# Performance work log

Measured on AMD Instinct MI355X. Metric: run time of the kernel, lower is better.

## Reference

```python
import jax, jax.numpy as jnp
import numpy as np

B, Nq, Nk, R = 4, 1024, 1024, 256
NH, DK, DV = 8, 64, 64


def setup_inputs() -> dict:
    key = jax.random.key(0)
    ks = jax.random.split(key, 16)
    mk = lambda k, shape, s=1.0: jax.random.normal(k, shape, dtype=jnp.float32) * s
    inp = {
        'Q_real': mk(ks[0], (B, Nq, R)), 'Q_imag': mk(ks[1], (B, Nq, R)),
        'K_real': mk(ks[2], (B, Nk, R)), 'K_imag': mk(ks[3], (B, Nk, R)),
        'V_real': mk(ks[4], (B, Nk, R)), 'V_imag': mk(ks[5], (B, Nk, R)),
        'WQ_r': mk(ks[6], (NH * DK, R), 0.02), 'WQ_i': mk(ks[7], (NH * DK, R), 0.02),
        'WK_r': mk(ks[8], (NH * DK, R), 0.02), 'WK_i': mk(ks[9], (NH * DK, R), 0.02),
        'WV_r': mk(ks[10], (NH * DV, R), 0.02), 'WV_i': mk(ks[11], (NH * DV, R), 0.02),
        'WO_r': mk(ks[12], (R, NH * DV), 0.02), 'WO_i': mk(ks[13], (R, NH * DV), 0.02),
        'mask': jax.random.randint(ks[14], (B, Nk), 0, 2).astype(bool),
    }
    return inp


def _complex_linear(x, w_r, w_i):
    # x: complex [..., in]; weights real [out, in]. Same math as 4 real matmuls.
    w = (w_r + 1j * w_i).astype(jnp.complex64)
    return x @ w.T


def reference(Q_real, Q_imag, K_real, K_imag, V_real, V_imag,
              WQ_r, WQ_i, WK_r, WK_i, WV_r, WV_i, WO_r, WO_i, mask):
    Q = (Q_real + 1j * Q_imag).astype(jnp.complex64)
    K = (K_real + 1j * K_imag).astype(jnp.complex64)
    V = (V_real + 1j * V_imag).astype(jnp.complex64)

    Qp = _complex_linear(Q, WQ_r, WQ_i).reshape(B, Nq, NH, DK).transpose(0, 2, 1, 3)
    Kp = _complex_linear(K, WK_r, WK_i).reshape(B, Nk, NH, DK).transpose(0, 2, 1, 3)
    Vp = _complex_linear(V, WV_r, WV_i).reshape(B, Nk, NH, DV).transpose(0, 2, 1, 3)

    # complex scores [B, NH, Nq, Nk]; conj on K matches torch .conj().transpose
    scores = jnp.einsum('bhqd,bhkd->bhqk', Qp, jnp.conj(Kp)) / jnp.sqrt(jnp.float32(DK))
    scores_abs = jnp.abs(scores)

    m = mask[:, None, None, :]                    # [B,1,1,Nk]
    valid = jnp.any(mask, axis=-1)[:, None, None, None]  # [B,1,1,1] valid query rows
    masked = jnp.where(m, scores_abs, -jnp.inf)
    # avoid all -inf rows feeding softmax (those rows are zeroed afterwards)
    safe = jnp.where(valid, masked, 0.0)
    w = jax.nn.softmax(safe, axis=-1)
    w = jnp.where(valid, w, 0.0)

    attn = jnp.einsum('bhqk,bhkd->bhqd', w.astype(Vp.dtype), Vp)
    attn = attn.transpose(0, 2, 1, 3).reshape(B, Nq, NH * DV)
    return _complex_linear(attn, WO_r, WO_i)
```

## Files before the change

### kernel.cpp

```cpp
#include <hip/hip_runtime.h>
#include <math.h>

#define NBATCH 4
#define NSEQ   1024
#define RD     256
#define NHEAD  8
#define HD     64
#define NHD    512

typedef __attribute__((ext_vector_type(8))) short  short8;
typedef __attribute__((ext_vector_type(4))) short  short4v;
typedef __attribute__((ext_vector_type(4))) float  float4v;

#define MFMA16(a,b,c) __builtin_amdgcn_mfma_f32_16x16x32_bf16(a,b,c,0,0,0)

typedef const void __attribute__((address_space(1)))* gas_t;
typedef void __attribute__((address_space(3)))* las_t;
#define GLOAD16(g, l) __builtin_amdgcn_global_load_lds((gas_t)(g), (las_t)(l), 16, 0, 0)

static __device__ __forceinline__ unsigned short f2b(float f) {
    union { float f; unsigned u; } x; x.f = f;
    unsigned r = x.u + 0x7fffu + ((x.u >> 16) & 1u);
    return (unsigned short)(r >> 16);
}
static __device__ __forceinline__ void st4(short* dst, float4v v) {
    short4v p;
    p[0] = (short)f2b(v[0]); p[1] = (short)f2b(v[1]);
    p[2] = (short)f2b(v[2]); p[3] = (short)f2b(v[3]);
    *(short4v*)dst = p;
}

struct ConvArgs { const float* src[15]; short* dst[15]; int n4[15]; };

__global__ __launch_bounds__(256) void convert_bf16(ConvArgs ca)
{
    const int a = blockIdx.y;
    if (a == 14) {
        if (blockIdx.x != 0) return;
        __shared__ int isByteLayout;
        const int t = threadIdx.x;
        if (t == 0) isByteLayout = 0;
        __syncthreads();
        const int* mi = (const int*)ca.src[14];
        #pragma unroll
        for (int j = 0; j < 4; j++) {
            int v = mi[t*4 + j];
            if (v & ~1) isByteLayout = 1;
        }
        __syncthreads();
        unsigned char* nm = (unsigned char*)ca.dst[14];
        const unsigned char* mb = (const unsigned char*)ca.src[14];
        if (isByteLayout) {
            #pragma unroll
            for (int j = 0; j < 16; j++) { int k = t*16 + j; nm[k] = mb[k] ? 1 : 0; }
        } else {
            #pragma unroll
            for (int j = 0; j < 16; j++) { int k = t*16 + j; nm[k] = mi[k] ? 1 : 0; }
        }
        return;
    }
    const float* __restrict__ s = ca.src[a];
    short* __restrict__ d = ca.dst[a];
    const int n4 = ca.n4[a];
    for (int i = blockIdx.x*256 + threadIdx.x; i < n4; i += gridDim.x*256) {
        float4v v = *(const float4v*)(s + (size_t)i*4);
        st4(d + (size_t)i*4, v);
    }
}

struct ProjArgs {
    const short* Xr[3]; const short* Xi[3];
    const short* Wr[3]; const short* Wi[3];
    short* Yr[3]; short* Yi[3];
};

__global__ __launch_bounds__(256) void cgemm_proj(ProjArgs pa)
{
    __shared__ short sX[2][128][64];
    __shared__ short sW[2][64][64];
    const int z = blockIdx.z;
    const short* __restrict__ X_r = pa.Xr[z];
    const short* __restrict__ X_i = pa.Xi[z];
    const short* __restrict__ W_r = pa.Wr[z];
    const short* __restrict__ W_i = pa.Wi[z];
    short* __restrict__ Y_r = pa.Yr[z];
    short* __restrict__ Y_i = pa.Yi[z];
    const int transposeOut = (z == 2);

    const int tid  = threadIdx.x;
    const int lane = tid & 63, wave = tid >> 6;
    const int quad = lane >> 4, l16 = lane & 15;
    const int sw8  = l16 & 7;
    const int rsub = lane >> 3;
    const int colg = (lane & 7) ^ rsub;
    const int n0 = blockIdx.x * 64, m0 = blockIdx.y * 128;

    const short nk = (short)0x8000;
    const short8 neg = {nk,nk,nk,nk,nk,nk,nk,nk};

    float4v zf = {0.f,0.f,0.f,0.f};
    float4v Yr[2][4], Yi[2][4];
    #pragma unroll
    for (int ms = 0; ms < 2; ms++)
        #pragma unroll
        for (int t = 0; t < 4; t++) { Yr[ms][t] = zf; Yi[ms][t] = zf; }

    for (int kc = 0; kc < RD; kc += 64) {
        __syncthreads();
        if (wave < 2) {
            const short* gp = wave ? X_i : X_r;
            short* lp = wave ? &sX[1][0][0] : &sX[0][0][0];
            #pragma unroll
            for (int j = 0; j < 16; j++) {
                int row = j*8 + rsub;
                GLOAD16(gp + (size_t)(m0 + row)*RD + kc + colg*8, lp + j*512);
            }
        } else {
            const short* gp = (wave == 3) ? W_i : W_r;
            short* lp = (wave == 3) ? &sW[1][0][0] : &sW[0][0][0];
            #pragma unroll
            for (int j = 0; j < 8; j++) {
                int row = j*8 + rsub;
                GLOAD16(gp + (size_t)(n0 + row)*RD + kc + colg*8, lp + j*512);
            }
        }
        __syncthreads();
        short8 fxr[2][2], fxi[2][2], fxin[2][2];
        #pragma unroll
        for (int ms = 0; ms < 2; ms++)
            #pragma unroll
            for (int ds = 0; ds < 2; ds++) {
                int row = wave*32 + ms*16 + l16;
                int u = ((ds*4 + quad) ^ sw8) * 8;
                fxr[ms][ds]  = *(short8*)&sX[0][row][u];
                fxi[ms][ds]  = *(short8*)&sX[1][row][u];
                fxin[ms][ds] = fxi[ms][ds] ^ neg;
            }
        #pragma unroll
        for (int t = 0; t < 4; t++)
            #pragma unroll
            for (int ds = 0; ds < 2; ds++) {
                int u = ((ds*4 + quad) ^ sw8) * 8;
                short8 wr = *(short8*)&sW[0][t*16 + l16][u];
                short8 wi = *(short8*)&sW[1][t*16 + l16][u];
                #pragma unroll
                for (int ms = 0; ms < 2; ms++) {
                    Yr[ms][t] = MFMA16(fxr[ms][ds],  wr, Yr[ms][t]);
                    Yr[ms][t] = MFMA16(fxin[ms][ds], wi, Yr[ms][t]);
                    Yi[ms][t] = MFMA16(fxr[ms][ds],  wi, Yi[ms][t]);
                    Yi[ms][t] = MFMA16(fxi[ms][ds],  wr, Yi[ms][t]);
                }
            }
    }

    const int b = m0 >> 10, h = n0 >> 6, nb = m0 & 1023;
    short* sT = &sX[0][0][0];
    short* Yp[2] = { Y_r, Y_i };
    #pragma unroll
    for (int p = 0; p < 2; p++) {
        __syncthreads();
        #pragma unroll
        for (int ms = 0; ms < 2; ms++)
            #pragma unroll
            for (int t = 0; t < 4; t++)
                #pragma unroll
                for (int r = 0; r < 4; r++) {
                    float v = p ? Yi[ms][t][r] : Yr[ms][t][r];
                    int rr = wave*32 + ms*16 + quad*4 + r;
                    int cc = t*16 + l16;
                    if (!transposeOut) sT[rr*68 + cc]  = (short)f2b(v);
                    else               sT[cc*132 + rr] = (short)f2b(v);
                }
        __syncthreads();
        #pragma unroll
        for (int it = 0; it < 4; it++) {
            int idx = it*256 + tid;
            int rr, c8;
            size_t o;
            const short* sp;
            if (!transposeOut) {
                rr = idx >> 3; c8 = (idx & 7)*8;
                sp = &sT[rr*68 + c8];
                o = (((size_t)(b*NHEAD + h))*NSEQ + nb + rr)*HD + c8;
            } else {
                rr = idx >> 4; c8 = (idx & 15)*8;
                sp = &sT[rr*132 + c8];
                o = (((size_t)(b*NHEAD + h))*HD + rr)*NSEQ + nb + c8;
            }
            short4v a = *(short4v*)sp;
            short4v bq = *(short4v*)(sp + 4);
            short8 v8 = { a[0],a[1],a[2],a[3], bq[0],bq[1],bq[2],bq[3] };
            *(short8*)&Yp[p][o] = v8;
        }
    }
}

__global__ __launch_bounds__(512) void attn_mfma(
    const short* __restrict__ Qp_r, const short* __restrict__ Qp_i,
    const short* __restrict__ Kp_r, const short* __restrict__ Kp_i,
    const short* __restrict__ Vp_r, const short* __restrict__ Vp_i,
    const unsigned char* __restrict__ mask,
    short* __restrict__ Ar, short* __restrict__ Ai)
{
    __shared__ __align__(16) char smem[76800];
    short (*sP)[16][40] = (short(*)[16][40])(smem + 65536);
    unsigned char* smask = (unsigned char*)(smem + 75776);

    const int tid  = threadIdx.x;
    const int lane = tid & 63, wave = tid >> 6;
    const int quad = lane >> 4, l16 = lane & 15;
    const int sw8  = l16 & 7;
    const int qstrip = wave >> 1;
    const int khalf  = wave & 1;
    const int qt = blockIdx.x >> 5;
    const int bh = blockIdx.x & 31;
    const int b  = bh >> 3, h = bh & 7;
    const size_t base = (size_t)bh * (NSEQ*HD);

    const int rsub = lane >> 3;
    const int colg = (lane & 7) ^ rsub;

    if (tid < 256) ((int*)smask)[tid] = ((const int*)(mask + b*NSEQ))[tid];

    const int splane = wave >> 1;
    const short* sgp = (splane == 0) ? Kp_r : (splane == 1) ? Kp_i
                     : (splane == 2) ? Vp_r : Vp_i;
    const int sisV = (splane >= 2);
    const int soff = splane * 8192;

    const short nk = (short)0x8000;
    const short8 neg = {nk,nk,nk,nk,nk,nk,nk,nk};
    short8 fqr[2], fqi[2], fqrn[2];
    #pragma unroll
    for (int ds = 0; ds < 2; ds++) {
        size_t qo = base + (size_t)(qt*64 + qstrip*16 + l16)*HD + ds*32 + quad*8;
        fqr[ds]  = *(const short8*)&Qp_r[qo];
        fqi[ds]  = *(const short8*)&Qp_i[qo];
        fqrn[ds] = fqr[ds] ^ neg;
    }

    float4v zf = {0.f,0.f,0.f,0.f};
    float4v Or[4], Oi[4];
    float lrow[4];
    #pragma unroll
    for (int t = 0; t < 4; t++) { Or[t] = zf; Oi[t] = zf; }
    #pragma unroll
    for (int r = 0; r < 4; r++) lrow[r] = 0.f;

    const float C2 = 0.18033688f;

    {
        short* lp = (short*)(smem + soff);
        #pragma unroll
        for (int jj = 0; jj < 4; jj++) {
            int j = (wave & 1)*4 + jj;
            int row = j*8 + rsub;
            const short* g = sisV
                ? sgp + base + (size_t)row*NSEQ + colg*8
                : sgp + base + (size_t)row*HD + colg*8;
            GLOAD16(g, lp + j*512);
        }
    }

    for (int kt = 0; kt < 16; kt++) {
        __syncthreads();

        if (kt + 1 < 16) {
            const int kn = (kt + 1) * 64;
            short* lp = (short*)(smem + ((kt + 1) & 1)*32768 + soff);
            #pragma unroll
            for (int jj = 0; jj < 4; jj++) {
                int j = (wave & 1)*4 + jj;
                int row = j*8 + rsub;
                const short* g = sisV
                    ? sgp + base + (size_t)row*NSEQ + kn + colg*8
                    : sgp + base + (size_t)(kn + row)*HD + colg*8;
                GLOAD16(g, lp + j*512);
            }
        }

        const char* buf = smem + (kt & 1)*32768;
        short (*sK0)[64] = (short(*)[64])(buf);
        short (*sK1)[64] = (short(*)[64])(buf + 8192);
        short (*sV0)[64] = (short(*)[64])(buf + 16384);
        short (*sV1)[64] = (short(*)[64])(buf + 24576);
        const int k0 = kt*64;

        float4v Sr[2], Si[2];
        Sr[0] = zf; Sr[1] = zf; Si[0] = zf; Si[1] = zf;
        #pragma unroll
        for (int t = 0; t < 2; t++)
            #pragma unroll
            for (int ds = 0; ds < 2; ds++) {
                int u = ((ds*4 + quad) ^ sw8) * 8;
                int krow = khalf*32 + t*16 + l16;
                short8 kr = *(short8*)&sK0[krow][u];
                short8 ki = *(short8*)&sK1[krow][u];
                Sr[t] = MFMA16(fqr[ds],  kr, Sr[t]);
                Sr[t] = MFMA16(fqi[ds],  ki, Sr[t]);
                Si[t] = MFMA16(fqi[ds],  kr, Si[t]);
                Si[t] = MFMA16(fqrn[ds], ki, Si[t]);
            }

        #pragma unroll
        for (int t = 0; t < 2; t++) {
            bool mv = smask[k0 + khalf*32 + t*16 + l16] != 0;
            #pragma unroll
            for (int r = 0; r < 4; r++) {
                float a = Sr[t][r], c = Si[t][r];
                float x = fmaf(a, a, c*c);
                float s = __builtin_amdgcn_sqrtf(x);
                float e = mv ? __builtin_amdgcn_exp2f(C2 * s) : 0.f;
                lrow[r] += e;
                sP[wave][quad*4 + r][t*16 + l16] = (short)f2b(e);
            }
        }

        {
            short8 fp = *(short8*)&sP[wave][l16][quad*8];
            #pragma unroll
            for (int t = 0; t < 4; t++) {
                int u = ((khalf*4 + quad) ^ sw8) * 8;
                short8 vr = *(short8*)&sV0[t*16 + l16][u];
                short8 vi = *(short8*)&sV1[t*16 + l16][u];
                Or[t] = MFMA16(fp, vr, Or[t]);
                Oi[t] = MFMA16(fp, vi, Oi[t]);
            }
        }
    }

    __syncthreads();
    float* sC = (float*)smem;
    float* sL = (float*)(smem + 32768);
    if (khalf == 1) {
        #pragma unroll
        for (int t = 0; t < 4; t++)
            #pragma unroll
            for (int r = 0; r < 4; r++) {
                int o8 = ((qstrip*4 + t)*64 + lane)*8 + r*2;
                sC[o8]     = Or[t][r];
                sC[o8 + 1] = Oi[t][r];
            }
        int lo = (qstrip*64 + lane)*4;
        #pragma unroll
        for (int r = 0; r < 4; r++) sL[lo + r] = lrow[r];
    }
    __syncthreads();
    if (khalf == 0) {
        #pragma unroll
        for (int t = 0; t < 4; t++)
            #pragma unroll
            for (int r = 0; r < 4; r++) {
                int o8 = ((qstrip*4 + t)*64 + lane)*8 + r*2;
                Or[t][r] += sC[o8];
                Oi[t][r] += sC[o8 + 1];
            }
        int lo = (qstrip*64 + lane)*4;
        float inv[4];
        #pragma unroll
        for (int r = 0; r < 4; r++) {
            float ls = lrow[r] + sL[lo + r];
            ls += __shfl_xor(ls, 1, 64);
            ls += __shfl_xor(ls, 2, 64);
            ls += __shfl_xor(ls, 4, 64);
            ls += __shfl_xor(ls, 8, 64);
            inv[r] = (ls > 0.f) ? 1.f/ls : 0.f;
        }
        #pragma unroll
        for (int t = 0; t < 4; t++)
            #pragma unroll
            for (int r = 0; r < 4; r++) {
                int q = qt*64 + qstrip*16 + quad*4 + r;
                int d = t*16 + l16;
                size_t o = ((size_t)(b*NSEQ + q))*NHD + h*HD + d;
                Ar[o] = (short)f2b(Or[t][r] * inv[r]);
                Ai[o] = (short)f2b(Oi[t][r] * inv[r]);
            }
    }
}

__global__ __launch_bounds__(256) void cgemm_out(
    const short* __restrict__ A_r, const short* __restrict__ A_i,
    const short* __restrict__ W_r, const short* __restrict__ W_i,
    float* __restrict__ Out, int writeImagPlane)
{
    __shared__ short sA[2][64][64];
    __shared__ short sW[2][32][64];
    const int tid  = threadIdx.x;
    const int lane = tid & 63, wave = tid >> 6;
    const int quad = lane >> 4, l16 = lane & 15;
    const int sw8  = l16 & 7;
    const int rsub = lane >> 3;
    const int colg = (lane & 7) ^ rsub;
    const int n0 = blockIdx.x * 32, m0 = blockIdx.y * 64;

    const short nk = (short)0x8000;
    const short8 neg = {nk,nk,nk,nk,nk,nk,nk,nk};

    float4v zf = {0.f,0.f,0.f,0.f};
    float4v Yr[2], Yi[2];
    #pragma unroll
    for (int t = 0; t < 2; t++) { Yr[t] = zf; Yi[t] = zf; }

    for (int kc = 0; kc < NHD; kc += 64) {
        __syncthreads();
        {
            if (wave < 2) {
                const short* gp = wave ? A_i : A_r;
                short* lp = wave ? &sA[1][0][0] : &sA[0][0][0];
                #pragma unroll
                for (int j = 0; j < 8; j++) {
                    int row = j*8 + rsub;
                    GLOAD16(gp + (size_t)(m0 + row)*NHD + kc + colg*8, lp + j*512);
                }
            } else {
                const short* gp = (wave == 3) ? W_i : W_r;
                short* lp = (wave == 3) ? &sW[1][0][0] : &sW[0][0][0];
                #pragma unroll
                for (int j = 0; j < 4; j++) {
                    int row = j*8 + rsub;
                    GLOAD16(gp + (size_t)(n0 + row)*NHD + kc + colg*8, lp + j*512);
                }
            }
        }
        __syncthreads();
        short8 far[2], fai[2], fain[2];
        #pragma unroll
        for (int ds = 0; ds < 2; ds++) {
            int u = ((ds*4 + quad) ^ sw8) * 8;
            far[ds]  = *(short8*)&sA[0][wave*16 + l16][u];
            fai[ds]  = *(short8*)&sA[1][wave*16 + l16][u];
            fain[ds] = fai[ds] ^ neg;
        }
        #pragma unroll
        for (int t = 0; t < 2; t++)
            #pragma unroll
            for (int ds = 0; ds < 2; ds++) {
                int u = ((ds*4 + quad) ^ sw8) * 8;
                short8 wr = *(short8*)&sW[0][t*16 + l16][u];
                short8 wi = *(short8*)&sW[1][t*16 + l16][u];
                Yr[t] = MFMA16(far[ds],  wr, Yr[t]);
                Yr[t] = MFMA16(fain[ds], wi, Yr[t]);
                Yi[t] = MFMA16(far[ds],  wi, Yi[t]);
                Yi[t] = MFMA16(fai[ds],  wr, Yi[t]);
            }
    }
    const size_t TOT = (size_t)NBATCH * NSEQ * RD;
    #pragma unroll
    for (int t = 0; t < 2; t++)
        #pragma unroll
        for (int r = 0; r < 4; r++) {
            int row = m0 + wave*16 + quad*4 + r;
            int col = n0 + t*16 + l16;
            size_t o = (size_t)row*RD + col;
            Out[o] = Yr[t][r];
            if (writeImagPlane) Out[o + TOT] = Yi[t][r];
        }
}

extern "C" void kernel_launch(void* const* d_in, const int* in_sizes, int n_in,
                              void* d_out, int out_size, void* d_ws, size_t ws_size,
                              hipStream_t stream)
{
    float* out = (float*)d_out;

    const size_t P = (size_t)NBATCH * NHEAD * NSEQ * HD;
    const size_t H = (size_t)NBATCH * NSEQ * RD;
    const size_t WSZ = (size_t)NHD * RD;

    short* bws = (short*)d_ws;
    short* Qpr = bws + 0*P;  short* Qpi = bws + 1*P;
    short* Kpr = bws + 2*P;  short* Kpi = bws + 3*P;
    short* Vpr = bws + 4*P;  short* Vpi = bws + 5*P;
    short* conv = bws + 6*P;
    short* cX[6]; for (int i = 0; i < 6; i++) cX[i] = conv + i*H;
    short* cW[6]; for (int i = 0; i < 6; i++) cW[i] = conv + 6*H + i*WSZ;
    short* cWOr = conv + 6*H + 6*WSZ;
    short* cWOi = conv + 6*H + 7*WSZ;
    short* Apr = conv;
    short* Api = conv + P;
    unsigned char* nmask = (unsigned char*)(conv + 6*H + 8*WSZ);

    const size_t TOT = (size_t)NBATCH * NSEQ * RD;
    const int writeImagPlane = ((size_t)out_size >= 2*TOT) ? 1 : 0;

    ConvArgs ca;
    for (int i = 0; i < 6; i++) {
        ca.src[i] = (const float*)d_in[i];  ca.dst[i] = cX[i];  ca.n4[i] = (int)(H/4);
    }
    for (int i = 0; i < 6; i++) {
        ca.src[6+i] = (const float*)d_in[6+i]; ca.dst[6+i] = cW[i]; ca.n4[6+i] = (int)(WSZ/4);
    }
    ca.src[12] = (const float*)d_in[12]; ca.dst[12] = cWOr; ca.n4[12] = (int)(WSZ/4);
    ca.src[13] = (const float*)d_in[13]; ca.dst[13] = cWOi; ca.n4[13] = (int)(WSZ/4);
    ca.src[14] = (const float*)d_in[14]; ca.dst[14] = (short*)nmask; ca.n4[14] = 0;

    ProjArgs pa;
    pa.Xr[0] = cX[0]; pa.Xi[0] = cX[1];
    pa.Xr[1] = cX[2]; pa.Xi[1] = cX[3];
    pa.Xr[2] = cX[4]; pa.Xi[2] = cX[5];
    pa.Wr[0] = cW[0]; pa.Wi[0] = cW[1];
    pa.Wr[1] = cW[2]; pa.Wi[1] = cW[3];
    pa.Wr[2] = cW[4]; pa.Wi[2] = cW[5];
    pa.Yr[0] = Qpr; pa.Yi[0] = Qpi;
    pa.Yr[1] = Kpr; pa.Yi[1] = Kpi;
    pa.Yr[2] = Vpr; pa.Yi[2] = Vpi;

    convert_bf16<<<dim3(256, 15), 256, 0, stream>>>(ca);
    cgemm_proj<<<dim3(8, 32, 3), 256, 0, stream>>>(pa);
    attn_mfma<<<dim3(512), 512, 0, stream>>>(Qpr, Qpi, Kpr, Kpi, Vpr, Vpi,
                                             nmask, Apr, Api);
    cgemm_out<<<dim3(8, 64), 256, 0, stream>>>(Apr, Api, cWOr, cWOi, out,
                                               writeImagPlane);
}
```

Baseline: 173.1 us.

## Halve attention block to 4 waves, each computing two 16-row query strips

The attention kernel now runs with 256 threads instead of 512. Each wave handles two 16-row query sub-strips and reuses every K and V fragment it reads from LDS across both. Each wave now loads a full plane of the K/V tile, so per-thread global-to-LDS load work doubles. Per-thread register use doubles for accumulators and Q fragments, and fewer waves per block reduces latency hiding.

```diff
diff --git a/kernel.cpp b/kernel.cpp
--- a/kernel.cpp
+++ b/kernel.cpp
@@ -195,7 +195,7 @@
     }
 }
 
-__global__ __launch_bounds__(512) void attn_mfma(
+__global__ __launch_bounds__(256) void attn_mfma(
     const short* __restrict__ Qp_r, const short* __restrict__ Qp_i,
     const short* __restrict__ Kp_r, const short* __restrict__ Kp_i,
     const short* __restrict__ Vp_r, const short* __restrict__ Vp_i,
@@ -203,15 +203,15 @@
     short* __restrict__ Ar, short* __restrict__ Ai)
 {
     __shared__ __align__(16) char smem[76800];
-    short (*sP)[16][40] = (short(*)[16][40])(smem + 65536);
+    short (*sP)[2][16][40] = (short(*)[2][16][40])(smem + 65536);
     unsigned char* smask = (unsigned char*)(smem + 75776);
 
     const int tid  = threadIdx.x;
     const int lane = tid & 63, wave = tid >> 6;
     const int quad = lane >> 4, l16 = lane & 15;
     const int sw8  = l16 & 7;
-    const int qstrip = wave >> 1;
-    const int khalf  = wave & 1;
+    const int qpair = wave >> 1;
+    const int khalf = wave & 1;
     const int qt = blockIdx.x >> 5;
     const int bh = blockIdx.x & 31;
     const int b  = bh >> 3, h = bh & 7;
@@ -220,40 +220,45 @@
     const int rsub = lane >> 3;
     const int colg = (lane & 7) ^ rsub;
 
-    if (tid < 256) ((int*)smask)[tid] = ((const int*)(mask + b*NSEQ))[tid];
-
-    const int splane = wave >> 1;
-    const short* sgp = (splane == 0) ? Kp_r : (splane == 1) ? Kp_i
-                     : (splane == 2) ? Vp_r : Vp_i;
-    const int sisV = (splane >= 2);
-    const int soff = splane * 8192;
+    ((int*)smask)[tid] = ((const int*)(mask + b*NSEQ))[tid];
+
+    const short* sgp = (wave == 0) ? Kp_r : (wave == 1) ? Kp_i
+                     : (wave == 2) ? Vp_r : Vp_i;
+    const int sisV = (wave >= 2);
+    const int soff = wave * 8192;
 
     const short nk = (short)0x8000;
     const short8 neg = {nk,nk,nk,nk,nk,nk,nk,nk};
-    short8 fqr[2], fqi[2], fqrn[2];
-    #pragma unroll
-    for (int ds = 0; ds < 2; ds++) {
-        size_t qo = base + (size_t)(qt*64 + qstrip*16 + l16)*HD + ds*32 + quad*8;
-        fqr[ds]  = *(const short8*)&Qp_r[qo];
-        fqi[ds]  = *(const short8*)&Qp_i[qo];
-        fqrn[ds] = fqr[ds] ^ neg;
-    }
+    short8 fqr[2][2], fqi[2][2], fqrn[2][2];
+    #pragma unroll
+    for (int qs = 0; qs < 2; qs++)
+        #pragma unroll
+        for (int ds = 0; ds < 2; ds++) {
+            size_t qo = base + (size_t)(qt*64 + qpair*32 + qs*16 + l16)*HD
+                             + ds*32 + quad*8;
+            fqr[qs][ds]  = *(const short8*)&Qp_r[qo];
+            fqi[qs][ds]  = *(const short8*)&Qp_i[qo];
+            fqrn[qs][ds] = fqr[qs][ds] ^ neg;
+        }
 
     float4v zf = {0.f,0.f,0.f,0.f};
-    float4v Or[4], Oi[4];
-    float lrow[4];
-    #pragma unroll
-    for (int t = 0; t < 4; t++) { Or[t] = zf; Oi[t] = zf; }
-    #pragma unroll
-    for (int r = 0; r < 4; r++) lrow[r] = 0.f;
+    float4v Or[2][4], Oi[2][4];
+    float lrow[2][4];
+    #pragma unroll
+    for (int qs = 0; qs < 2; qs++)
+        #pragma unroll
+        for (int t = 0; t < 4; t++) { Or[qs][t] = zf; Oi[qs][t] = zf; }
+    #pragma unroll
+    for (int qs = 0; qs < 2; qs++)
+        #pragma unroll
+        for (int r = 0; r < 4; r++) lrow[qs][r] = 0.f;
 
     const float C2 = 0.18033688f;
 
     {
         short* lp = (short*)(smem + soff);
         #pragma unroll
-        for (int jj = 0; jj < 4; jj++) {
-            int j = (wave & 1)*4 + jj;
+        for (int j = 0; j < 8; j++) {
             int row = j*8 + rsub;
             const short* g = sisV
                 ? sgp + base + (size_t)row*NSEQ + colg*8
@@ -269,8 +274,7 @@
             const int kn = (kt + 1) * 64;
             short* lp = (short*)(smem + ((kt + 1) & 1)*32768 + soff);
             #pragma unroll
-            for (int jj = 0; jj < 4; jj++) {
-                int j = (wave & 1)*4 + jj;
+            for (int j = 0; j < 8; j++) {
                 int row = j*8 + rsub;
                 const short* g = sisV
                     ? sgp + base + (size_t)row*NSEQ + kn + colg*8
@@ -286,8 +290,12 @@
         short (*sV1)[64] = (short(*)[64])(buf + 24576);
         const int k0 = kt*64;
 
-        float4v Sr[2], Si[2];
-        Sr[0] = zf; Sr[1] = zf; Si[0] = zf; Si[1] = zf;
+        float4v Sr[2][2], Si[2][2];
+        #pragma unroll
+        for (int qs = 0; qs < 2; qs++) {
+            Sr[qs][0] = zf; Sr[qs][1] = zf;
+            Si[qs][0] = zf; Si[qs][1] = zf;
+        }
         #pragma unroll
         for (int t = 0; t < 2; t++)
             #pragma unroll
@@ -296,35 +304,46 @@
                 int krow = khalf*32 + t*16 + l16;
                 short8 kr = *(short8*)&sK0[krow][u];
                 short8 ki = *(short8*)&sK1[krow][u];
-                Sr[t] = MFMA16(fqr[ds],  kr, Sr[t]);
-                Sr[t] = MFMA16(fqi[ds],  ki, Sr[t]);
-                Si[t] = MFMA16(fqi[ds],  kr, Si[t]);
-                Si[t] = MFMA16(fqrn[ds], ki, Si[t]);
+                #pragma unroll
+                for (int qs = 0; qs < 2; qs++) {
+                    Sr[qs][t] = MFMA16(fqr[qs][ds],  kr, Sr[qs][t]);
+                    Sr[qs][t] = MFMA16(fqi[qs][ds],  ki, Sr[qs][t]);
+                    Si[qs][t] = MFMA16(fqi[qs][ds],  kr, Si[qs][t]);
+                    Si[qs][t] = MFMA16(fqrn[qs][ds], ki, Si[qs][t]);
+                }
             }
 
         #pragma unroll
         for (int t = 0; t < 2; t++) {
             bool mv = smask[k0 + khalf*32 + t*16 + l16] != 0;
             #pragma unroll
-            for (int r = 0; r < 4; r++) {
-                float a = Sr[t][r], c = Si[t][r];
-                float x = fmaf(a, a, c*c);
-                float s = __builtin_amdgcn_sqrtf(x);
-                float e = mv ? __builtin_amdgcn_exp2f(C2 * s) : 0.f;
-                lrow[r] += e;
-                sP[wave][quad*4 + r][t*16 + l16] = (short)f2b(e);
-            }
+            for (int qs = 0; qs < 2; qs++)
+                #pragma unroll
+                for (int r = 0; r < 4; r++) {
+                    float a = Sr[qs][t][r], c = Si[qs][t][r];
+                    float x = fmaf(a, a, c*c);
+                    float s = __builtin_amdgcn_sqrtf(x);
+                    float e = mv ? __builtin_amdgcn_exp2f(C2 * s) : 0.f;
+                    lrow[qs][r] += e;
+                    sP[wave][qs][quad*4 + r][t*16 + l16] = (short)f2b(e);
+                }
         }
 
         {
-            short8 fp = *(short8*)&sP[wave][l16][quad*8];
+            short8 fp[2];
+            #pragma unroll
+            for (int qs = 0; qs < 2; qs++)
+                fp[qs] = *(short8*)&sP[wave][qs][l16][quad*8];
             #pragma unroll
             for (int t = 0; t < 4; t++) {
                 int u = ((khalf*4 + quad) ^ sw8) * 8;
                 short8 vr = *(short8*)&sV0[t*16 + l16][u];
                 short8 vi = *(short8*)&sV1[t*16 + l16][u];
-                Or[t] = MFMA16(fp, vr, Or[t]);
-                Oi[t] = MFMA16(fp, vi, Oi[t]);
+                #pragma unroll
+                for (int qs = 0; qs < 2; qs++) {
+                    Or[qs][t] = MFMA16(fp[qs], vr, Or[qs][t]);
+                    Oi[qs][t] = MFMA16(fp[qs], vi, Oi[qs][t]);
+                }
             }
         }
     }
@@ -334,48 +353,54 @@
     float* sL = (float*)(smem + 32768);
     if (khalf == 1) {
         #pragma unroll
-        for (int t = 0; t < 4; t++)
-            #pragma unroll
-            for (int r = 0; r < 4; r++) {
-                int o8 = ((qstrip*4 + t)*64 + lane)*8 + r*2;
-                sC[o8]     = Or[t][r];
-                sC[o8 + 1] = Oi[t][r];
-            }
-        int lo = (qstrip*64 + lane)*4;
-        #pragma unroll
-        for (int r = 0; r < 4; r++) sL[lo + r] = lrow[r];
+        for (int qs = 0; qs < 2; qs++) {
+            #pragma unroll
+            for (int t = 0; t < 4; t++)
+                #pragma unroll
+                for (int r = 0; r < 4; r++) {
+                    int o8 = (((qpair*2 + qs)*4 + t)*64 + lane)*8 + r*2;
+                    sC[o8]     = Or[qs][t][r];
+                    sC[o8 + 1] = Oi[qs][t][r];
+                }
+            int lo = ((qpair*2 + qs)*64 + lane)*4;
+            #pragma unroll
+            for (int r = 0; r < 4; r++) sL[lo + r] = lrow[qs][r];
+        }
     }
     __syncthreads();
     if (khalf == 0) {
         #pragma unroll
-        for (int t = 0; t < 4; t++)
+        for (int qs = 0; qs < 2; qs++) {
+            #pragma unroll
+            for (int t = 0; t < 4; t++)
+                #pragma unroll
+                for (int r = 0; r < 4; r++) {
+                    int o8 = (((qpair*2 + qs)*4 + t)*64 + lane)*8 + r*2;
+                    Or[qs][t][r] += sC[o8];
+                    Oi[qs][t][r] += sC[o8 + 1];
+                }
+            int lo = ((qpair*2 + qs)*64 + lane)*4;
+            float inv[4];
             #pragma unroll
             for (int r = 0; r < 4; r++) {
-                int o8 = ((qstrip*4 + t)*64 + lane)*8 + r*2;
-                Or[t][r] += sC[o8];
-                Oi[t][r] += sC[o8 + 1];
-            }
-        int lo = (qstrip*64 + lane)*4;
-        float inv[4];
-        #pragma unroll
-        for (int r = 0; r < 4; r++) {
-            float ls = lrow[r] + sL[lo + r];
-            ls += __shfl_xor(ls, 1, 64);
-            ls += __shfl_xor(ls, 2, 64);
-            ls += __shfl_xor(ls, 4, 64);
-            ls += __shfl_xor(ls, 8, 64);
-            inv[r] = (ls > 0.f) ? 1.f/ls : 0.f;
-        }
-        #pragma unroll
-        for (int t = 0; t < 4; t++)
-            #pragma unroll
-            for (int r = 0; r < 4; r++) {
-                int q = qt*64 + qstrip*16 + quad*4 + r;
-                int d = t*16 + l16;
-                size_t o = ((size_t)(b*NSEQ + q))*NHD + h*HD + d;
-                Ar[o] = (short)f2b(Or[t][r] * inv[r]);
-                Ai[o] = (short)f2b(Oi[t][r] * inv[r]);
-            }
+                float ls = lrow[qs][r] + sL[lo + r];
+                ls += __shfl_xor(ls, 1, 64);
+                ls += __shfl_xor(ls, 2, 64);
+                ls += __shfl_xor(ls, 4, 64);
+                ls += __shfl_xor(ls, 8, 64);
+                inv[r] = (ls > 0.f) ? 1.f/ls : 0.f;
+            }
+            #pragma unroll
+            for (int t = 0; t < 4; t++)
+                #pragma unroll
+                for (int r = 0; r < 4; r++) {
+                    int q = qt*64 + qpair*32 + qs*16 + quad*4 + r;
+                    int d = t*16 + l16;
+                    size_t o = ((size_t)(b*NSEQ + q))*NHD + h*HD + d;
+                    Ar[o] = (short)f2b(Or[qs][t][r] * inv[r]);
+                    Ai[o] = (short)f2b(Oi[qs][t][r] * inv[r]);
+                }
+        }
     }
 }
 
@@ -508,7 +533,7 @@
 
     convert_bf16<<<dim3(256, 15), 256, 0, stream>>>(ca);
     cgemm_proj<<<dim3(8, 32, 3), 256, 0, stream>>>(pa);
-    attn_mfma<<<dim3(512), 512, 0, stream>>>(Qpr, Qpi, Kpr, Kpi, Vpr, Vpi,
+    attn_mfma<<<dim3(512), 256, 0, stream>>>(Qpr, Qpi, Kpr, Kpi, Vpr, Vpi,
                                              nmask, Apr, Api);
     cgemm_out<<<dim3(8, 64), 256, 0, stream>>>(Apr, Api, cWOr, cWOi, out,
                                                writeImagPlane);
```

Measured after the change: 176.4 us. No clear change (+1.9%).
